# Kernel tuning notes

Measured on AMD Instinct MI355X. Metric: run time of the kernel, lower is better.

Reference implementation:

```python
import jax, jax.numpy as jnp
import numpy as np
import math

NUM_HEADS = 16
KEY_DIM = 64
MODEL_DIM = 1024
NEG_INF = -1000000000.0


def _get_slopes(n):
    def pow2_slopes(n):
        start = 2 ** (-2 ** (-(math.log2(n) - 3)))
        return [start * start ** i for i in range(n)]
    if math.log2(n).is_integer():
        s = pow2_slopes(n)
    else:
        c = 2 ** math.floor(math.log2(n))
        s = pow2_slopes(c) + pow2_slopes(2 * c)[0::2][: n - c]
    return jnp.asarray(s, dtype=jnp.float32)


def setup_inputs() -> dict:
    key = jax.random.key(0)
    ks = jax.random.split(key, 11)
    B, S, D = 4, 2048, MODEL_DIM
    P = NUM_HEADS * KEY_DIM
    sd = 1.0 / math.sqrt(D)
    return {
        "query": jax.random.normal(ks[0], (B, S, D), jnp.float32),
        "key": jax.random.normal(ks[1], (B, S, D), jnp.float32),
        "value": jax.random.normal(ks[2], (B, S, D), jnp.float32),
        "Wq": jax.random.normal(ks[3], (D, P), jnp.float32) * sd,
        "bq": jnp.zeros((P,), jnp.float32),
        "Wk": jax.random.normal(ks[4], (D, P), jnp.float32) * sd,
        "bk": jnp.zeros((P,), jnp.float32),
        "Wv": jax.random.normal(ks[5], (D, P), jnp.float32) * sd,
        "bv": jnp.zeros((P,), jnp.float32),
        "Wo": jax.random.normal(ks[6], (P, D), jnp.float32) * (1.0 / math.sqrt(P)),
        "bo": jnp.zeros((D,), jnp.float32),
    }


def reference(query, key, value, Wq, bq, Wk, bk, Wv, bv, Wo, bo):
    B, S, _ = query.shape
    H, Kd = NUM_HEADS, KEY_DIM

    def split_heads(x):  # [B,S,H*Kd] -> [B,H,S,Kd]
        return x.reshape(B, S, H, Kd).transpose(0, 2, 1, 3)

    q = split_heads(query @ Wq + bq)
    k = split_heads(key @ Wk + bk)
    v = split_heads(value @ Wv + bv)

    logits = jnp.einsum("bhqd,bhkd->bhqk", q, k) / jnp.sqrt(jnp.float32(Kd))

    i = jnp.arange(S)[:, None]
    j = jnp.arange(S)[None, :]
    causal = jnp.where(i >= j, 0.0, NEG_INF).astype(jnp.float32)  # [S,S]
    rel = (i - j).astype(jnp.float32)  # [S,S]
    slopes = _get_slopes(H)  # [H]
    alibi = slopes[:, None, None] * rel  # [H,S,S]
    logits = logits + causal[None, None, :, :] + alibi[None, :, :, :]

    weights = jax.nn.softmax(logits, axis=-1)
    attn = jnp.einsum("bhqk,bhkd->bhqd", weights, v)
    concat = attn.transpose(0, 2, 1, 3).reshape(B, S, H * Kd)
    return concat @ Wo + bo
```

## Files before the change

kernel.cpp:

```cpp
#include <hip/hip_runtime.h>

#define B_ 4
#define S_ 2048
#define D_ 1024
#define H_ 16
#define KD_ 64
#define P_ 1024
#define M_ (B_*S_)

typedef unsigned short u16;
typedef unsigned int u32;
typedef __attribute__((ext_vector_type(2))) unsigned u32x2;
typedef __attribute__((ext_vector_type(4))) float f32x4;
typedef __attribute__((ext_vector_type(8))) __bf16 bf16x8;

__device__ __forceinline__ u16 f2bf(float f) {
  u32 x = __float_as_uint(f);
  return (u16)((x + 0x7fffu + ((x >> 16) & 1u)) >> 16);
}

__device__ __forceinline__ void gl_lds16(const u16* g, u16* l) {
  __builtin_amdgcn_global_load_lds((__attribute__((address_space(1))) void*)g,
                                   (__attribute__((address_space(3))) void*)l, 16, 0, 0);
}

__device__ __forceinline__ u32 pkbf(float a, float b) {
  return __builtin_amdgcn_perm(__float_as_uint(b) + 0x8000u,
                               __float_as_uint(a) + 0x8000u, 0x07060302u);
}

#if __has_builtin(__builtin_amdgcn_permlane32_swap) && __has_builtin(__builtin_amdgcn_permlane16_swap)
__device__ __forceinline__ void plswap(u32& a, u32& b) {
  u32x2 r32 = __builtin_amdgcn_permlane32_swap(a, b, false, false);
  u32x2 r16 = __builtin_amdgcn_permlane16_swap(r32[0], r32[1], false, false);
  a = r16[0]; b = r16[1];
}
#else
__device__ __forceinline__ void plswap(u32& a, u32& b) {
  const int l = threadIdx.x & 63;
  const int quad = l >> 4, l16 = l & 15;
  int i0 = (((quad & 1) * 32) + l16) * 4;
  int i1 = i0 + 64;
  int a_lo = __builtin_amdgcn_ds_bpermute(i0, (int)a);
  int b_lo = __builtin_amdgcn_ds_bpermute(i0, (int)b);
  int a_hi = __builtin_amdgcn_ds_bpermute(i1, (int)a);
  int b_hi = __builtin_amdgcn_ds_bpermute(i1, (int)b);
  u32 na = (quad < 2) ? (u32)a_lo : (u32)b_lo;
  u32 nb = (quad < 2) ? (u32)a_hi : (u32)b_hi;
  a = na; b = nb;
}
#endif

__global__ void cvt3_kernel(const float* __restrict__ q, const float* __restrict__ k,
                            const float* __restrict__ v,
                            u16* __restrict__ Xq, u16* __restrict__ Xk, u16* __restrict__ Xv) {
  const int z = blockIdx.y;
  const float* in = z == 0 ? q : z == 1 ? k : v;
  u16* out = z == 0 ? Xq : z == 1 ? Xk : Xv;
  int i = blockIdx.x * 256 + threadIdx.x;
  float4 vv = ((const float4*)in)[i];
  ((u32*)out)[i*2+0] = (u32)f2bf(vv.x) | ((u32)f2bf(vv.y) << 16);
  ((u32*)out)[i*2+1] = (u32)f2bf(vv.z) | ((u32)f2bf(vv.w) << 16);
}

__global__ void transpose_cvt4(const float* __restrict__ Wq, const float* __restrict__ Wk,
                               const float* __restrict__ Wv, const float* __restrict__ Wo,
                               u16* __restrict__ WqT, u16* __restrict__ WkT,
                               u16* __restrict__ WvT, u16* __restrict__ WoT) {
  const int z = blockIdx.z;
  const float* in = z == 0 ? Wq : z == 1 ? Wk : z == 2 ? Wv : Wo;
  u16* out = z == 0 ? WqT : z == 1 ? WkT : z == 2 ? WvT : WoT;
  __shared__ float tile[32][33];
  int bx = blockIdx.x * 32, by = blockIdx.y * 32;
  int tx = threadIdx.x, ty = threadIdx.y;
  #pragma unroll
  for (int kk = 0; kk < 4; ++kk)
    tile[ty + kk*8][tx] = in[(by + ty + kk*8) * 1024 + bx + tx];
  __syncthreads();
  #pragma unroll
  for (int kk = 0; kk < 4; ++kk)
    out[(bx + ty + kk*8) * 1024 + by + tx] = f2bf(tile[tx][ty + kk*8]);
}

__global__ __launch_bounds__(256) void gemm_qkv(
    const u16* __restrict__ Xq, const u16* __restrict__ Xk, const u16* __restrict__ Xv,
    const u16* __restrict__ WqT, const u16* __restrict__ WkT, const u16* __restrict__ WvT,
    const float* __restrict__ bq, const float* __restrict__ bk, const float* __restrict__ bv,
    u16* __restrict__ Qb, u16* __restrict__ Kb, u16* __restrict__ Vt)
{
  constexpr int K = 1024, N = 1024, BK = 32;
  const int z = blockIdx.z;
  const u16* A  = z == 0 ? Xq  : z == 1 ? Xk  : Xv;
  const u16* Bt = z == 0 ? WqT : z == 1 ? WkT : WvT;
  const float* bias = z == 0 ? bq : z == 1 ? bk : bv;

  __shared__ alignas(16) u16 As[128*BK];
  __shared__ alignas(16) u16 Bs[128*BK];
  const int tid = threadIdx.x;
  const int w = tid >> 6, l = tid & 63;
  const int quad = l >> 4, l16 = l & 15;
  const int wm = (w >> 1) * 64, wn = (w & 1) * 64;
  const long mBase = (long)blockIdx.x * 128;
  const int  nBase = blockIdx.y * 128;

  f32x4 acc[4][4] = {};
  const int off0 = w*1024 + l*16;

  for (int kb = 0; kb < K/BK; ++kb) {
    __syncthreads();
    #pragma unroll
    for (int p = 0; p < 2; ++p) {
      int off = p*4096 + off0;
      int row = off >> 6;
      int cb  = off & 63;
      const u16* ga = A  + (mBase + row)*K + kb*BK + (cb >> 1);
      const u16* gb = Bt + ((long)(nBase + row))*K + kb*BK + (cb >> 1);
      gl_lds16(ga, (u16*)((char*)As + p*4096 + w*1024));
      gl_lds16(gb, (u16*)((char*)Bs + p*4096 + w*1024));
    }
    __syncthreads();
    bf16x8 af[4], bf[4];
    #pragma unroll
    for (int i = 0; i < 4; ++i) af[i] = *(const bf16x8*)&As[(wm + i*16 + l16)*BK + quad*8];
    #pragma unroll
    for (int j = 0; j < 4; ++j) bf[j] = *(const bf16x8*)&Bs[(wn + j*16 + l16)*BK + quad*8];
    #pragma unroll
    for (int i = 0; i < 4; ++i)
      #pragma unroll
      for (int j = 0; j < 4; ++j)
        acc[i][j] = __builtin_amdgcn_mfma_f32_16x16x32_bf16(af[i], bf[j], acc[i][j], 0, 0, 0);
  }

  if (z < 2) {
    u16* Cout = z == 0 ? Qb : Kb;
    #pragma unroll
    for (int i = 0; i < 4; ++i)
      #pragma unroll
      for (int j = 0; j < 4; ++j)
        #pragma unroll
        for (int r = 0; r < 4; ++r) {
          long row = mBase + wm + i*16 + quad*4 + r;
          int  col = nBase + wn + j*16 + l16;
          Cout[row*N + col] = f2bf(acc[i][j][r] + bias[col]);
        }
  } else {
    #pragma unroll
    for (int i = 0; i < 4; ++i)
      #pragma unroll
      for (int j = 0; j < 4; ++j) {
        int  col  = nBase + wn + j*16 + l16;
        long row0 = mBase + wm + i*16 + quad*4;
        int  bb = (int)(row0 >> 11);
        int  ss = (int)(row0 & 2047);
        float bcol = bias[col];
        float v0 = acc[i][j][0] + bcol, v1 = acc[i][j][1] + bcol;
        float v2 = acc[i][j][2] + bcol, v3 = acc[i][j][3] + bcol;
        uint2 pk;
        pk.x = (u32)f2bf(v0) | ((u32)f2bf(v1) << 16);
        pk.y = (u32)f2bf(v2) | ((u32)f2bf(v3) << 16);
        *(uint2*)&Vt[((long)(bb*16) * 64 + col) * 2048 + ss] = pk;
      }
  }
}

__global__ __launch_bounds__(256) void gemm_out(const u16* __restrict__ A,
                                                const u16* __restrict__ Bt,
                                                const float* __restrict__ bias,
                                                float* __restrict__ Cout)
{
  constexpr int K = 1024, N = 1024, BK = 32;
  __shared__ alignas(16) u16 As[128*BK];
  __shared__ alignas(16) u16 Bs[128*BK];
  const int tid = threadIdx.x;
  const int w = tid >> 6, l = tid & 63;
  const int quad = l >> 4, l16 = l & 15;
  const int wm = (w >> 1) * 64, wn = (w & 1) * 64;
  const long mBase = (long)blockIdx.x * 128;
  const int  nBase = blockIdx.y * 128;

  f32x4 acc[4][4] = {};
  const int off0 = w*1024 + l*16;

  for (int kb = 0; kb < K/BK; ++kb) {
    __syncthreads();
    #pragma unroll
    for (int p = 0; p < 2; ++p) {
      int off = p*4096 + off0;
      int row = off >> 6;
      int cb  = off & 63;
      const u16* ga = A  + (mBase + row)*K + kb*BK + (cb >> 1);
      const u16* gb = Bt + ((long)(nBase + row))*K + kb*BK + (cb >> 1);
      gl_lds16(ga, (u16*)((char*)As + p*4096 + w*1024));
      gl_lds16(gb, (u16*)((char*)Bs + p*4096 + w*1024));
    }
    __syncthreads();
    bf16x8 af[4], bf[4];
    #pragma unroll
    for (int i = 0; i < 4; ++i) af[i] = *(const bf16x8*)&As[(wm + i*16 + l16)*BK + quad*8];
    #pragma unroll
    for (int j = 0; j < 4; ++j) bf[j] = *(const bf16x8*)&Bs[(wn + j*16 + l16)*BK + quad*8];
    #pragma unroll
    for (int i = 0; i < 4; ++i)
      #pragma unroll
      for (int j = 0; j < 4; ++j)
        acc[i][j] = __builtin_amdgcn_mfma_f32_16x16x32_bf16(af[i], bf[j], acc[i][j], 0, 0, 0);
  }

  #pragma unroll
  for (int i = 0; i < 4; ++i)
    #pragma unroll
    for (int j = 0; j < 4; ++j)
      #pragma unroll
      for (int r = 0; r < 4; ++r) {
        long row = mBase + wm + i*16 + quad*4 + r;
        int  col = nBase + wn + j*16 + l16;
        Cout[row*N + col] = acc[i][j][r] + bias[col];
      }
}

__global__ __launch_bounds__(128, 2) void attn_kernel(const u16* __restrict__ Qb,
                                                      const u16* __restrict__ Kb,
                                                      const u16* __restrict__ Vt,
                                                      u16* __restrict__ Ob)
{
  const int n = blockIdx.x;
  const int qt = 15 - (n >> 6);
  const int r6 = n & 63;
  const int b = r6 >> 4, h = r6 & 15;
  const int w = threadIdx.x >> 6;
  const int l = threadIdx.x & 63;
  const int quad = l >> 4, l16 = l & 15;
  const float LOG2E = 1.44269504089f;
  const float slope = exp2f(-0.5f * (float)(h + 1));
  const float c1  = 0.125f * LOG2E;
  const float sl2 = slope * LOG2E;
  const float rs1 = sl2, rs2 = 2.f*sl2, rs3 = 3.f*sl2;

  const int q0 = qt*128 + w*64;
  const u16* Qp = Qb + ((long)(b*S_ + q0))*P_ + h*KD_;
  const u16* Kp = Kb + ((long)(b*S_))*P_ + h*KD_;
  const u16* Vp = Vt + ((long)(b*H_ + h))*KD_*S_;

  bf16x8 qf[4][2];
  #pragma unroll
  for (int i = 0; i < 4; ++i)
    #pragma unroll
    for (int kk = 0; kk < 2; ++kk)
      qf[i][kk] = *(const bf16x8*)&Qp[(long)(i*16 + l16)*P_ + kk*32 + quad*8];

  f32x4 o[4][4] = {};
  float lsum[4] = {0.f, 0.f, 0.f, 0.f};

  auto kissue = [&](int it, bf16x8& k00, bf16x8& k01, bf16x8& k10, bf16x8& k11) {
    const int kt = it >> 2, ks = it & 3;
    const u16* kp = Kp + (long)(kt*128 + l16 + 2*ks*16)*P_;
    k00 = *(const bf16x8*)(kp + quad*8);
    k01 = *(const bf16x8*)(kp + 32 + quad*8);
    k10 = *(const bf16x8*)(kp + 16*P_ + quad*8);
    k11 = *(const bf16x8*)(kp + 16*P_ + 32 + quad*8);
  };
  auto compute = [&](int it, const bf16x8& k00, const bf16x8& k01,
                     const bf16x8& k10, const bf16x8& k11) {
    const int kt = it >> 2, ks = it & 3;
    const u16* vp = Vp + (long)l16*S_ + kt*128 + ks*32 + quad*8;
    bf16x8 v0 = *(const bf16x8*)(vp);
    bf16x8 v1 = *(const bf16x8*)(vp + 16*S_);
    bf16x8 v2 = *(const bf16x8*)(vp + 32*S_);
    bf16x8 v3 = *(const bf16x8*)(vp + 48*S_);
    const float kb0 = (float)(kt*128 + 2*ks*16 + quad*4);
    u32 pw0[4][2], pw1[4][2];
    {
      const float bij = -sl2 * kb0;
      #pragma unroll
      for (int i = 0; i < 4; ++i) {
        f32x4 t = {};
        t = __builtin_amdgcn_mfma_f32_16x16x32_bf16(k00, qf[i][0], t, 0, 0, 0);
        t = __builtin_amdgcn_mfma_f32_16x16x32_bf16(k01, qf[i][1], t, 0, 0, 0);
        float p0 = __builtin_amdgcn_exp2f(fmaf(t[0], c1, bij));
        float p1 = __builtin_amdgcn_exp2f(fmaf(t[1], c1, bij) - rs1);
        float p2 = __builtin_amdgcn_exp2f(fmaf(t[2], c1, bij) - rs2);
        float p3 = __builtin_amdgcn_exp2f(fmaf(t[3], c1, bij) - rs3);
        lsum[i] += (p0 + p1) + (p2 + p3);
        pw0[i][0] = pkbf(p0, p1);
        pw0[i][1] = pkbf(p2, p3);
      }
    }
    {
      const float bij = -sl2 * (kb0 + 16.f);
      #pragma unroll
      for (int i = 0; i < 4; ++i) {
        f32x4 t = {};
        t = __builtin_amdgcn_mfma_f32_16x16x32_bf16(k10, qf[i][0], t, 0, 0, 0);
        t = __builtin_amdgcn_mfma_f32_16x16x32_bf16(k11, qf[i][1], t, 0, 0, 0);
        float p0 = __builtin_amdgcn_exp2f(fmaf(t[0], c1, bij));
        float p1 = __builtin_amdgcn_exp2f(fmaf(t[1], c1, bij) - rs1);
        float p2 = __builtin_amdgcn_exp2f(fmaf(t[2], c1, bij) - rs2);
        float p3 = __builtin_amdgcn_exp2f(fmaf(t[3], c1, bij) - rs3);
        lsum[i] += (p0 + p1) + (p2 + p3);
        pw1[i][0] = pkbf(p0, p1);
        pw1[i][1] = pkbf(p2, p3);
      }
    }
    #pragma unroll
    for (int i = 0; i < 4; ++i) {
      u32 fa0 = pw0[i][0], fb0 = pw1[i][0];
      u32 fa1 = pw0[i][1], fb1 = pw1[i][1];
      plswap(fa0, fb0);
      plswap(fa1, fb1);
      union { u32 u[4]; bf16x8 v; } fu;
      fu.u[0] = fa0; fu.u[1] = fa1; fu.u[2] = fb0; fu.u[3] = fb1;
      const bf16x8 pb = fu.v;
      o[i][0] = __builtin_amdgcn_mfma_f32_16x16x32_bf16(v0, pb, o[i][0], 0, 0, 0);
      o[i][1] = __builtin_amdgcn_mfma_f32_16x16x32_bf16(v1, pb, o[i][1], 0, 0, 0);
      o[i][2] = __builtin_amdgcn_mfma_f32_16x16x32_bf16(v2, pb, o[i][2], 0, 0, 0);
      o[i][3] = __builtin_amdgcn_mfma_f32_16x16x32_bf16(v3, pb, o[i][3], 0, 0, 0);
    }
  };

  const int nit = qt * 4;
  if (nit > 0) {
    bf16x8 ak00, ak01, ak10, ak11;
    bf16x8 bk00, bk01, bk10, bk11;
    kissue(0, ak00, ak01, ak10, ak11);
    int it = 0;
    while (true) {
      if (it + 1 < nit) kissue(it + 1, bk00, bk01, bk10, bk11);
      compute(it, ak00, ak01, ak10, ak11);
      ++it; if (it == nit) break;
      if (it + 1 < nit) kissue(it + 1, ak00, ak01, ak10, ak11);
      compute(it, bk00, bk01, bk10, bk11);
      ++it; if (it == nit) break;
    }
  }

  {
    const int kt = qt;
    const int ksmax = 2*w + 2;
    const u16* kts = Kp + (long)(kt*128 + l16)*P_;
    for (int ks = 0; ks < ksmax; ++ks) {
      const u16* vp = Vp + (long)l16*S_ + kt*128 + ks*32 + quad*8;
      bf16x8 v0 = *(const bf16x8*)(vp);
      bf16x8 v1 = *(const bf16x8*)(vp + 16*S_);
      bf16x8 v2 = *(const bf16x8*)(vp + 32*S_);
      bf16x8 v3 = *(const bf16x8*)(vp + 48*S_);
      u32 pw[4][2][2];
      #pragma unroll
      for (int jp = 0; jp < 2; ++jp) {
        const int j = 2*ks + jp;
        const u16* kp = kts + (long)(j*16)*P_;
        bf16x8 kf0 = *(const bf16x8*)(kp + quad*8);
        bf16x8 kf1 = *(const bf16x8*)(kp + 32 + quad*8);
        const int kl0 = j*16 + quad*4;
        const float bij = -sl2 * (float)(kt*128 + kl0);
        #pragma unroll
        for (int i = 0; i < 4; ++i) {
          const int ql = w*64 + i*16 + l16;
          f32x4 t = {};
          t = __builtin_amdgcn_mfma_f32_16x16x32_bf16(kf0, qf[i][0], t, 0, 0, 0);
          t = __builtin_amdgcn_mfma_f32_16x16x32_bf16(kf1, qf[i][1], t, 0, 0, 0);
          float x0 = fmaf(t[0], c1, bij);
          float x1 = fmaf(t[1], c1, bij) - rs1;
          float x2 = fmaf(t[2], c1, bij) - rs2;
          float x3 = fmaf(t[3], c1, bij) - rs3;
          if (kl0 + 0 > ql) x0 = -1e30f;
          if (kl0 + 1 > ql) x1 = -1e30f;
          if (kl0 + 2 > ql) x2 = -1e30f;
          if (kl0 + 3 > ql) x3 = -1e30f;
          float p0 = __builtin_amdgcn_exp2f(x0);
          float p1 = __builtin_amdgcn_exp2f(x1);
          float p2 = __builtin_amdgcn_exp2f(x2);
          float p3 = __builtin_amdgcn_exp2f(x3);
          lsum[i] += (p0 + p1) + (p2 + p3);
          pw[i][jp][0] = pkbf(p0, p1);
          pw[i][jp][1] = pkbf(p2, p3);
        }
      }
      #pragma unroll
      for (int i = 0; i < 4; ++i) {
        u32 fa0 = pw[i][0][0], fb0 = pw[i][1][0];
        u32 fa1 = pw[i][0][1], fb1 = pw[i][1][1];
        plswap(fa0, fb0);
        plswap(fa1, fb1);
        union { u32 u[4]; bf16x8 v; } fu;
        fu.u[0] = fa0; fu.u[1] = fa1; fu.u[2] = fb0; fu.u[3] = fb1;
        const bf16x8 pb = fu.v;
        o[i][0] = __builtin_amdgcn_mfma_f32_16x16x32_bf16(v0, pb, o[i][0], 0, 0, 0);
        o[i][1] = __builtin_amdgcn_mfma_f32_16x16x32_bf16(v1, pb, o[i][1], 0, 0, 0);
        o[i][2] = __builtin_amdgcn_mfma_f32_16x16x32_bf16(v2, pb, o[i][2], 0, 0, 0);
        o[i][3] = __builtin_amdgcn_mfma_f32_16x16x32_bf16(v3, pb, o[i][3], 0, 0, 0);
      }
    }
  }

  #pragma unroll
  for (int i = 0; i < 4; ++i) {
    lsum[i] += __shfl_xor(lsum[i], 16, 64);
    lsum[i] += __shfl_xor(lsum[i], 32, 64);
    const float inv = 1.0f / lsum[i];
    #pragma unroll
    for (int jn = 0; jn < 4; ++jn) {
      float v0 = o[i][jn][0] * inv, v1 = o[i][jn][1] * inv;
      float v2 = o[i][jn][2] * inv, v3 = o[i][jn][3] * inv;
      uint2 pk;
      pk.x = (u32)f2bf(v0) | ((u32)f2bf(v1) << 16);
      pk.y = (u32)f2bf(v2) | ((u32)f2bf(v3) << 16);
      *(uint2*)&Ob[((long)(b*S_ + q0 + i*16 + l16))*P_ + h*KD_ + jn*16 + quad*4] = pk;
    }
  }
}

extern "C" void kernel_launch(void* const* d_in, const int* in_sizes, int n_in,
                              void* d_out, int out_size, void* d_ws, size_t ws_size,
                              hipStream_t stream) {
  const float* q  = (const float*)d_in[0];
  const float* k  = (const float*)d_in[1];
  const float* v  = (const float*)d_in[2];
  const float* Wq = (const float*)d_in[3];
  const float* bq = (const float*)d_in[4];
  const float* Wk = (const float*)d_in[5];
  const float* bk = (const float*)d_in[6];
  const float* Wv = (const float*)d_in[7];
  const float* bv = (const float*)d_in[8];
  const float* Wo = (const float*)d_in[9];
  const float* bo = (const float*)d_in[10];

  const size_t X_ELEMS = (size_t)M_ * P_;
  const size_t W_ELEMS = (size_t)D_ * P_;
  u16* ws  = (u16*)d_ws;
  u16* Xq  = ws;
  u16* Xk  = Xq  + X_ELEMS;
  u16* Xv  = Xk  + X_ELEMS;
  u16* WqT = Xv  + X_ELEMS;
  u16* WkT = WqT + W_ELEMS;
  u16* WvT = WkT + W_ELEMS;
  u16* WoT = WvT + W_ELEMS;
  u16* Qb  = WoT + W_ELEMS;
  u16* Kb  = Qb  + X_ELEMS;
  u16* Vt  = Kb  + X_ELEMS;
  u16* Attn = Xq;

  cvt3_kernel<<<dim3((unsigned)(X_ELEMS/4/256), 3), 256, 0, stream>>>(q, k, v, Xq, Xk, Xv);

  transpose_cvt4<<<dim3(32, 32, 4), dim3(32, 8), 0, stream>>>(Wq, Wk, Wv, Wo,
                                                              WqT, WkT, WvT, WoT);

  gemm_qkv<<<dim3(M_/128, P_/128, 3), 256, 0, stream>>>(Xq, Xk, Xv, WqT, WkT, WvT,
                                                        bq, bk, bv, Qb, Kb, Vt);

  attn_kernel<<<dim3(1024), 128, 0, stream>>>(Qb, Kb, Vt, Attn);

  gemm_out<<<dim3(M_/128, P_/128), 256, 0, stream>>>(Attn, WoT, bo, (float*)d_out);
}
```

Measured before the change: 341.0 us.

## Split attention KV range across two waves per query tile and merge via LDS

Doubles the attention block to 256 threads so that each 64-row query group gets two waves, each covering half of the off-diagonal key tiles. The second wave also handles the diagonal tile. The partial output accumulators and row sums are merged through shared memory before normalisation and the bf16 store. Merging without a max rescale is valid because the softmax here uses no running max. This adds parallelism to the attention phase but costs 32KB+ of LDS, a block-wide sync, and an uneven split where the diagonal work lands on one wave.

```diff
diff --git a/kernel.cpp b/kernel.cpp
--- a/kernel.cpp
+++ b/kernel.cpp
@@ -218,7 +218,7 @@
       }
 }
 
-__global__ __launch_bounds__(128, 2) void attn_kernel(const u16* __restrict__ Qb,
+__global__ __launch_bounds__(256, 2) void attn_kernel(const u16* __restrict__ Qb,
                                                       const u16* __restrict__ Kb,
                                                       const u16* __restrict__ Vt,
                                                       u16* __restrict__ Ob)
@@ -227,7 +227,8 @@
   const int qt = 15 - (n >> 6);
   const int r6 = n & 63;
   const int b = r6 >> 4, h = r6 & 15;
-  const int w = threadIdx.x >> 6;
+  const int wq = threadIdx.x >> 7;
+  const int wk = (threadIdx.x >> 6) & 1;
   const int l = threadIdx.x & 63;
   const int quad = l >> 4, l16 = l & 15;
   const float LOG2E = 1.44269504089f;
@@ -236,7 +237,7 @@
   const float sl2 = slope * LOG2E;
   const float rs1 = sl2, rs2 = 2.f*sl2, rs3 = 3.f*sl2;
 
-  const int q0 = qt*128 + w*64;
+  const int q0 = qt*128 + wq*64;
   const u16* Qp = Qb + ((long)(b*S_ + q0))*P_ + h*KD_;
   const u16* Kp = Kb + ((long)(b*S_))*P_ + h*KD_;
   const u16* Vp = Vt + ((long)(b*H_ + h))*KD_*S_;
@@ -317,25 +318,27 @@
     }
   };
 
-  const int nit = qt * 4;
-  if (nit > 0) {
+  const int split = (qt + 1) >> 1;
+  const int itLo = wk ? split*4 : 0;
+  const int itHi = wk ? qt*4 : split*4;
+  if (itHi > itLo) {
     bf16x8 ak00, ak01, ak10, ak11;
     bf16x8 bk00, bk01, bk10, bk11;
-    kissue(0, ak00, ak01, ak10, ak11);
-    int it = 0;
+    kissue(itLo, ak00, ak01, ak10, ak11);
+    int it = itLo;
     while (true) {
-      if (it + 1 < nit) kissue(it + 1, bk00, bk01, bk10, bk11);
+      if (it + 1 < itHi) kissue(it + 1, bk00, bk01, bk10, bk11);
       compute(it, ak00, ak01, ak10, ak11);
-      ++it; if (it == nit) break;
-      if (it + 1 < nit) kissue(it + 1, ak00, ak01, ak10, ak11);
+      ++it; if (it == itHi) break;
+      if (it + 1 < itHi) kissue(it + 1, ak00, ak01, ak10, ak11);
       compute(it, bk00, bk01, bk10, bk11);
-      ++it; if (it == nit) break;
-    }
-  }
-
-  {
+      ++it; if (it == itHi) break;
+    }
+  }
+
+  if (wk) {
     const int kt = qt;
-    const int ksmax = 2*w + 2;
+    const int ksmax = 2*wq + 2;
     const u16* kts = Kp + (long)(kt*128 + l16)*P_;
     for (int ks = 0; ks < ksmax; ++ks) {
       const u16* vp = Vp + (long)l16*S_ + kt*128 + ks*32 + quad*8;
@@ -354,7 +357,7 @@
         const float bij = -sl2 * (float)(kt*128 + kl0);
         #pragma unroll
         for (int i = 0; i < 4; ++i) {
-          const int ql = w*64 + i*16 + l16;
+          const int ql = wq*64 + i*16 + l16;
           f32x4 t = {};
           t = __builtin_amdgcn_mfma_f32_16x16x32_bf16(kf0, qf[i][0], t, 0, 0, 0);
           t = __builtin_amdgcn_mfma_f32_16x16x32_bf16(kf1, qf[i][1], t, 0, 0, 0);
@@ -392,19 +395,44 @@
     }
   }
 
-  #pragma unroll
-  for (int i = 0; i < 4; ++i) {
-    lsum[i] += __shfl_xor(lsum[i], 16, 64);
-    lsum[i] += __shfl_xor(lsum[i], 32, 64);
-    const float inv = 1.0f / lsum[i];
-    #pragma unroll
-    for (int jn = 0; jn < 4; ++jn) {
-      float v0 = o[i][jn][0] * inv, v1 = o[i][jn][1] * inv;
-      float v2 = o[i][jn][2] * inv, v3 = o[i][jn][3] * inv;
-      uint2 pk;
-      pk.x = (u32)f2bf(v0) | ((u32)f2bf(v1) << 16);
-      pk.y = (u32)f2bf(v2) | ((u32)f2bf(v3) << 16);
-      *(uint2*)&Ob[((long)(b*S_ + q0 + i*16 + l16))*P_ + h*KD_ + jn*16 + quad*4] = pk;
+  __shared__ float Lo[2][4][4][4][64];
+  __shared__ float Ls[2][4][64];
+  if (!wk) {
+    #pragma unroll
+    for (int i = 0; i < 4; ++i) {
+      #pragma unroll
+      for (int jn = 0; jn < 4; ++jn)
+        #pragma unroll
+        for (int r = 0; r < 4; ++r)
+          Lo[wq][i][jn][r][l] = o[i][jn][r];
+      Ls[wq][i][l] = lsum[i];
+    }
+  }
+  __syncthreads();
+  if (wk) {
+    #pragma unroll
+    for (int i = 0; i < 4; ++i) {
+      #pragma unroll
+      for (int jn = 0; jn < 4; ++jn)
+        #pragma unroll
+        for (int r = 0; r < 4; ++r)
+          o[i][jn][r] += Lo[wq][i][jn][r][l];
+      lsum[i] += Ls[wq][i][l];
+    }
+    #pragma unroll
+    for (int i = 0; i < 4; ++i) {
+      lsum[i] += __shfl_xor(lsum[i], 16, 64);
+      lsum[i] += __shfl_xor(lsum[i], 32, 64);
+      const float inv = 1.0f / lsum[i];
+      #pragma unroll
+      for (int jn = 0; jn < 4; ++jn) {
+        float v0 = o[i][jn][0] * inv, v1 = o[i][jn][1] * inv;
+        float v2 = o[i][jn][2] * inv, v3 = o[i][jn][3] * inv;
+        uint2 pk;
+        pk.x = (u32)f2bf(v0) | ((u32)f2bf(v1) << 16);
+        pk.y = (u32)f2bf(v2) | ((u32)f2bf(v3) << 16);
+        *(uint2*)&Ob[((long)(b*S_ + q0 + i*16 + l16))*P_ + h*KD_ + jn*16 + quad*4] = pk;
+      }
     }
   }
 }
@@ -447,7 +475,7 @@
   gemm_qkv<<<dim3(M_/128, P_/128, 3), 256, 0, stream>>>(Xq, Xk, Xv, WqT, WkT, WvT,
                                                         bq, bk, bv, Qb, Kb, Vt);
 
-  attn_kernel<<<dim3(1024), 128, 0, stream>>>(Qb, Kb, Vt, Attn);
+  attn_kernel<<<dim3(1024), 256, 0, stream>>>(Qb, Kb, Vt, Attn);
 
   gemm_out<<<dim3(M_/128, P_/128), 256, 0, stream>>>(Attn, WoT, bo, (float*)d_out);
 }
```

Measured after the change: 333.9 us. 1.02x faster.
